# Kernel tuning notes

Hardware: AMD Instinct MI355X
Metric: run time of the kernel (lower is better)

Reference implementation:

```python
import jax, jax.numpy as jnp
import numpy as np

DIM = 1024
HEADS = 8


def setup_inputs() -> dict:
    key = jax.random.key(0)
    ks = jax.random.split(key, 8)
    b, n, m, nc, d = 2, 1024, 4, 1024, DIM
    x = jax.random.normal(ks[0], (b, n, d), dtype=jnp.float32)
    context = jax.random.normal(ks[1], (b, m, nc, d), dtype=jnp.float32)
    doc_similarities = jax.random.normal(ks[2], (b, m), dtype=jnp.float32)
    # learned params (Linear weights stored as [in, out] for x @ W)
    s = 1.0 / np.sqrt(d)
    Wq = jax.random.uniform(ks[3], (d, d), minval=-s, maxval=s, dtype=jnp.float32)
    Wkv = jax.random.uniform(ks[4], (d, 2 * d), minval=-s, maxval=s, dtype=jnp.float32)
    Wout = jax.random.uniform(ks[5], (d, d), minval=-s, maxval=s, dtype=jnp.float32)
    bout = jax.random.uniform(ks[6], (d,), minval=-s, maxval=s, dtype=jnp.float32)
    beta = jnp.array(1.0, dtype=jnp.float32)
    return {"x": x, "context": context, "doc_similarities": doc_similarities,
            "Wq": Wq, "Wkv": Wkv, "beta": beta, "Wout": Wout, "bout": bout}


def reference(x, context, doc_similarities, Wq, Wkv, beta, Wout, bout):
    b, n, dim = x.shape
    h = HEADS
    hd = dim // h
    scale = dim ** -0.5
    m, nc = context.shape[1], context.shape[2]

    # q: [b, h, n, hd]
    q = (x @ Wq).reshape(b, n, h, hd).transpose(0, 2, 1, 3)

    # flatten docs: [b, m*nc, dim]
    ctx = context.reshape(b, m * nc, dim)
    # doc similarity bias, repeated per token within each doc: [b, m*nc]
    sim = jnp.repeat(doc_similarities, nc, axis=1) * beta

    kv = ctx @ Wkv  # [b, L, 2*dim]
    k, v = jnp.split(kv, 2, axis=-1)
    k = k.reshape(b, m * nc, h, hd).transpose(0, 2, 1, 3)  # [b, h, L, hd]
    v = v.reshape(b, m * nc, h, hd).transpose(0, 2, 1, 3)

    dots = jnp.einsum('bhid,bhjd->bhij', q, k) * scale
    dots = dots + sim[:, None, None, :]
    attn = jax.nn.softmax(dots, axis=-1)
    out = jnp.einsum('bhij,bhjd->bhid', attn, v)
    out = out.transpose(0, 2, 1, 3).reshape(b, n, dim)
    return out @ Wout + bout
```

## Files before the change

### kernel.cpp

```cpp
#include <hip/hip_runtime.h>
#include <stdint.h>

typedef __attribute__((ext_vector_type(4))) float f32x4;
typedef __attribute__((ext_vector_type(8))) __bf16 bf16x8;

__device__ __forceinline__ uint16_t f2bf(float f) {
  uint32_t u = __builtin_bit_cast(uint32_t, f);
  u += 0x7FFFu + ((u >> 16) & 1u);
  return (uint16_t)(u >> 16);
}

__device__ __forceinline__ float bf2f(uint16_t u) {
  uint32_t v = ((uint32_t)u) << 16;
  return __builtin_bit_cast(float, v);
}

__device__ __forceinline__ void load_lds16(const uint16_t* g, uint16_t* l) {
  __builtin_amdgcn_global_load_lds((const __attribute__((address_space(1))) void*)g,
                                   (__attribute__((address_space(3))) void*)l, 16, 0, 0);
}

__global__ __launch_bounds__(256) void k_prep(const float* __restrict__ x,
                                              const float* __restrict__ ctx,
                                              const float* __restrict__ Wq,
                                              const float* __restrict__ Wkv,
                                              const float* __restrict__ Wout,
                                              uint16_t* __restrict__ xb,
                                              uint16_t* __restrict__ ctxb,
                                              uint16_t* __restrict__ wqt,
                                              uint16_t* __restrict__ wkvt,
                                              uint16_t* __restrict__ woutt,
                                              float qscale) {
  __shared__ float tile[32][33];
  int id = blockIdx.x;
  int tid = threadIdx.x;
  if (id < 10240) {
    const float* in;
    uint16_t* out;
    int j = id * 256 + tid;
    if (j < 524288) { in = x; out = xb; }
    else            { in = ctx; out = ctxb; j -= 524288; }
    float4 v = ((const float4*)in)[j];
    union { uint16_t u[4]; uint64_t q; } o;
    o.u[0] = f2bf(v.x); o.u[1] = f2bf(v.y); o.u[2] = f2bf(v.z); o.u[3] = f2bf(v.w);
    ((uint64_t*)out)[j] = o.q;
    return;
  }
  id -= 10240;
  const float* W;
  uint16_t* Wt;
  int N, n0, k0;
  float sc = 1.0f;
  if (id < 1024)      { W = Wq;   Wt = wqt;   N = 1024; sc = qscale;
                        n0 = (id & 31) * 32; k0 = (id >> 5) * 32; }
  else if (id < 2048) { W = Wout; Wt = woutt; N = 1024; id -= 1024;
                        n0 = (id & 31) * 32; k0 = (id >> 5) * 32; }
  else                { W = Wkv;  Wt = wkvt;  N = 2048; id -= 2048;
                        n0 = (id & 63) * 32; k0 = (id >> 6) * 32; }
  int c = tid & 31, r0 = tid >> 5;
#pragma unroll
  for (int i = 0; i < 4; i++) {
    int r = r0 + i * 8;
    tile[r][c] = W[(size_t)(k0 + r) * N + n0 + c];
  }
  __syncthreads();
#pragma unroll
  for (int i = 0; i < 4; i++) {
    int r = r0 + i * 8;
    Wt[(size_t)(n0 + r) * 1024 + k0 + c] = f2bf(tile[c][r] * sc);
  }
}

__global__ __launch_bounds__(256) void k_gemm_fused(const uint16_t* __restrict__ ctxb,
                                                    const uint16_t* __restrict__ wkvt,
                                                    const uint16_t* __restrict__ xb,
                                                    const uint16_t* __restrict__ wqt,
                                                    uint16_t* __restrict__ kb,
                                                    uint16_t* __restrict__ vtb,
                                                    uint16_t* __restrict__ qb) {
  __shared__ uint16_t smem[9216];
  uint16_t* la = smem;
  uint16_t* lb = smem + 4096;
  const int K = 1024;
  const int tid = threadIdx.x;
  const int lane = tid & 63, w = tid >> 6;
  const int quad = lane >> 4, l16 = lane & 15;
  const int wr = (w >> 1) * 64, wc = (w & 1) * 64;
  int id = blockIdx.x;
  int bx, by, isQ;
  const uint16_t *Ab, *Bb;
  if (id < 1024) {
    isQ = 0; bx = id & 15; by = id >> 4;
    Ab = ctxb + (size_t)by * 128 * K;
    Bb = wkvt + (size_t)bx * 128 * K;
  } else {
    isQ = 1; id -= 1024; bx = id & 7; by = id >> 3;
    Ab = xb + (size_t)by * 128 * K;
    Bb = wqt + (size_t)bx * 128 * K;
  }
  f32x4 acc[4][4] = {};
  const int rA = tid >> 2, slotA = tid & 3;
  const int rA1 = rA + 64;
  const int segA0 = (slotA ^ ((rA + (rA >> 2)) & 3)) * 8;
  const int segA1 = (slotA ^ ((rA1 + (rA1 >> 2)) & 3)) * 8;
  for (int k0 = 0; k0 < K; k0 += 32) {
    __syncthreads();
    load_lds16(Ab + (size_t)rA * K + k0 + segA0, la + tid * 8);
    load_lds16(Ab + (size_t)rA1 * K + k0 + segA1, la + (tid + 256) * 8);
    load_lds16(Bb + (size_t)rA * K + k0 + segA0, lb + tid * 8);
    load_lds16(Bb + (size_t)rA1 * K + k0 + segA1, lb + (tid + 256) * 8);
    __syncthreads();
    bf16x8 af[4], bfr[4];
#pragma unroll
    for (int i = 0; i < 4; i++) {
      int R = wr + i * 16 + l16;
      int s = quad ^ ((R + (R >> 2)) & 3);
      af[i] = *(const bf16x8*)&la[R * 32 + s * 8];
    }
#pragma unroll
    for (int j = 0; j < 4; j++) {
      int R = wc + j * 16 + l16;
      int s = quad ^ ((R + (R >> 2)) & 3);
      bfr[j] = *(const bf16x8*)&lb[R * 32 + s * 8];
    }
#pragma unroll
    for (int i = 0; i < 4; i++)
#pragma unroll
      for (int j = 0; j < 4; j++)
        acc[i][j] = __builtin_amdgcn_mfma_f32_16x16x32_bf16(af[i], bfr[j], acc[i][j], 0, 0, 0);
  }
  __syncthreads();
  if (isQ) {
#pragma unroll
    for (int i = 0; i < 4; i++)
#pragma unroll
      for (int j = 0; j < 4; j++) {
        size_t row = (size_t)by * 128 + wr + i * 16 + quad * 4;
        size_t col = (size_t)bx * 128 + wc + j * 16 + l16;
#pragma unroll
        for (int r = 0; r < 4; r++)
          qb[(row + r) * 1024 + col] = f2bf(acc[i][j][r]);
      }
  } else if (bx < 8) {
#pragma unroll
    for (int i = 0; i < 4; i++)
#pragma unroll
      for (int j = 0; j < 4; j++) {
        size_t row = (size_t)by * 128 + wr + i * 16 + quad * 4;
        size_t col = (size_t)bx * 128 + wc + j * 16 + l16;
#pragma unroll
        for (int r = 0; r < 4; r++)
          kb[(row + r) * 1024 + col] = f2bf(acc[i][j][r]);
      }
  } else {
    const int bh = (by >> 5) * 8 + (bx - 8);
    const int lbase = (by & 31) * 128;
    uint16_t* vdst = vtb + (size_t)bh * 524288;
#pragma unroll
    for (int half = 0; half < 2; half++) {
      if (wr == half * 64) {
#pragma unroll
        for (int i = 0; i < 4; i++)
#pragma unroll
          for (int j = 0; j < 4; j++) {
            int rowl = i * 16 + quad * 4;
            int col = wc + j * 16 + l16;
            union { uint64_t q; uint16_t u[4]; } pk;
#pragma unroll
            for (int r = 0; r < 4; r++) pk.u[r] = f2bf(acc[i][j][r]);
            *(uint64_t*)&smem[col * 72 + rowl] = pk.q;
          }
      }
      __syncthreads();
      {
        int col = tid >> 1, rseg = (tid & 1) * 32;
        const uint16_t* src = &smem[col * 72 + rseg];
        uint16_t* d = vdst + (size_t)col * 4096 + lbase + half * 64 + rseg;
#pragma unroll
        for (int k = 0; k < 4; k++)
          ((uint4*)d)[k] = *(const uint4*)&src[k * 8];
      }
      __syncthreads();
    }
  }
}

__global__ __launch_bounds__(256) void k_gemm64(const uint16_t* __restrict__ A,
                                                const uint16_t* __restrict__ Bt,
                                                float* __restrict__ Cf,
                                                const float* __restrict__ bias,
                                                int M, int N, int K) {
  __shared__ uint16_t la[64 * 64];
  __shared__ uint16_t lb[64 * 64];
  const int tid = threadIdx.x;
  const int lane = tid & 63, w = tid >> 6;
  const int quad = lane >> 4, l16 = lane & 15;
  const int wr = (w >> 1) * 32, wc = (w & 1) * 32;
  const size_t tr0 = (size_t)blockIdx.y * 64, tc0 = (size_t)blockIdx.x * 64;
  f32x4 acc[2][2] = {};
  const int rS = tid >> 3, sS = tid & 7;
  const int seg = (sS ^ (rS & 7)) * 8;
  const uint16_t* Ab = A + tr0 * K;
  const uint16_t* Bb = Bt + tc0 * K;
  for (int k0 = 0; k0 < K; k0 += 64) {
    __syncthreads();
    load_lds16(Ab + (size_t)rS * K + k0 + seg, la + tid * 8);
    load_lds16(Ab + (size_t)(rS + 32) * K + k0 + seg, la + (tid + 256) * 8);
    load_lds16(Bb + (size_t)rS * K + k0 + seg, lb + tid * 8);
    load_lds16(Bb + (size_t)(rS + 32) * K + k0 + seg, lb + (tid + 256) * 8);
    __syncthreads();
#pragma unroll
    for (int sub = 0; sub < 2; sub++) {
      const int kk = sub * 4 + quad;
      bf16x8 af[2], bfr[2];
#pragma unroll
      for (int i = 0; i < 2; i++) {
        int R = wr + i * 16 + l16;
        af[i] = *(const bf16x8*)&la[R * 64 + (kk ^ (R & 7)) * 8];
      }
#pragma unroll
      for (int j = 0; j < 2; j++) {
        int R = wc + j * 16 + l16;
        bfr[j] = *(const bf16x8*)&lb[R * 64 + (kk ^ (R & 7)) * 8];
      }
#pragma unroll
      for (int i = 0; i < 2; i++)
#pragma unroll
        for (int j = 0; j < 2; j++)
          acc[i][j] = __builtin_amdgcn_mfma_f32_16x16x32_bf16(af[i], bfr[j], acc[i][j], 0, 0, 0);
    }
  }
#pragma unroll
  for (int i = 0; i < 2; i++) {
#pragma unroll
    for (int j = 0; j < 2; j++) {
      size_t row = tr0 + wr + i * 16 + quad * 4;
      size_t col = tc0 + wc + j * 16 + l16;
#pragma unroll
      for (int r = 0; r < 4; r++)
        Cf[(row + r) * N + col] = acc[i][j][r] + bias[col];
    }
  }
}

__global__ __launch_bounds__(256) void k_attn(const uint16_t* __restrict__ q,
                                              const uint16_t* __restrict__ kb,
                                              const uint16_t* __restrict__ vt,
                                              const float* __restrict__ sims,
                                              const float* __restrict__ beta,
                                              uint16_t* __restrict__ po,
                                              float* __restrict__ pm,
                                              float* __restrict__ pl) {
  __shared__ uint16_t Kl[2][8192];
  __shared__ uint16_t Vl[2][8192];
  __shared__ uint16_t Pl[4 * 2048];
  const int bz = blockIdx.z, b = bz >> 2, sp = bz & 3;
  const int h = blockIdx.y, q0 = blockIdx.x * 128;
  const int tid = threadIdx.x, lane = tid & 63, w = tid >> 6;
  const int quad = lane >> 4, l16 = lane & 15;
  const float simv_l2 = sims[b * 4 + sp] * beta[0] * 1.44269504f;
  uint16_t* Pw = Pl + w * 2048;

  union { uint32_t u[4]; bf16x8 v; } Oc;
#pragma unroll
  for (int j = 0; j < 4; j++) Oc.u[j] = 0x3F803F80u;
  const bf16x8 onesf = Oc.v;

  bf16x8 qf[2][4];
#pragma unroll
  for (int rb = 0; rb < 2; rb++) {
    const uint16_t* qrow =
        q + ((size_t)(b * 1024 + q0 + w * 32 + rb * 16 + l16)) * 1024 + h * 128 + quad * 8;
#pragma unroll
    for (int ks = 0; ks < 4; ks++) qf[rb][ks] = *(const bf16x8*)(qrow + ks * 32);
  }
  f32x4 o[2][8] = {};
  f32x4 o9[2] = {};

  const uint16_t* kbase = kb + ((size_t)(b * 4096 + sp * 1024)) * 1024 + h * 128;
  const uint16_t* vbase = vt + ((size_t)(b * 8 + h) * 128) * 4096 + sp * 1024;

  auto stage = [&](int c, int bi) {
    const uint16_t* kc = kbase + (size_t)c * 64 * 1024;
    const uint16_t* vc = vbase + c * 64;
    uint16_t* Kb = Kl[bi];
    uint16_t* Vb = Vl[bi];
#pragma unroll
    for (int ii = 0; ii < 4; ii++) {
      int g = tid + ii * 256;
      int row = g >> 4, seg = (g & 15) ^ (row & 15);
      load_lds16(kc + (size_t)row * 1024 + seg * 8, Kb + g * 8);
    }
#pragma unroll
    for (int ii = 0; ii < 4; ii++) {
      int g = tid + ii * 256;
      int row = g >> 3, seg = (g & 7) ^ (row & 7);
      load_lds16(vc + (size_t)row * 4096 + seg * 8, Vb + g * 8);
    }
  };

  stage(0, 0);
  for (int c = 0; c < 16; c++) {
    __syncthreads();
    if (c < 15) stage(c + 1, (c + 1) & 1);
    const uint16_t* Kb = Kl[c & 1];
    const uint16_t* Vb = Vl[c & 1];
#pragma unroll
    for (int nb = 0; nb < 4; nb++) {
      f32x4 s0 = {}, s1 = {};
#pragma unroll
      for (int ks = 0; ks < 4; ks++) {
        bf16x8 kf = *(const bf16x8*)&Kb[(nb * 16 + l16) * 128 + (((ks * 4 + quad) ^ l16) * 8)];
        s0 = __builtin_amdgcn_mfma_f32_16x16x32_bf16(qf[0][ks], kf, s0, 0, 0, 0);
        s1 = __builtin_amdgcn_mfma_f32_16x16x32_bf16(qf[1][ks], kf, s1, 0, 0, 0);
      }
      const int s_lin = nb * 2 + (l16 >> 3);
#pragma unroll
      for (int r = 0; r < 4; r++) {
        int rp0 = quad * 4 + r;
        Pw[rp0 * 64 + ((s_lin ^ (rp0 & 7)) * 8) + (l16 & 7)] =
            f2bf(__builtin_amdgcn_exp2f(s0[r]));
        int rp1 = 16 + rp0;
        Pw[rp1 * 64 + ((s_lin ^ (rp1 & 7)) * 8) + (l16 & 7)] =
            f2bf(__builtin_amdgcn_exp2f(s1[r]));
      }
    }
    __asm__ volatile("s_waitcnt lgkmcnt(0)" ::: "memory");
#pragma unroll
    for (int ks = 0; ks < 2; ks++) {
      const int sq = ((ks * 4 + quad) ^ (l16 & 7)) * 8;
      bf16x8 pf0 = *(const bf16x8*)&Pw[l16 * 64 + sq];
      bf16x8 pf1 = *(const bf16x8*)&Pw[(16 + l16) * 64 + sq];
#pragma unroll
      for (int nb = 0; nb < 8; nb++) {
        bf16x8 vf = *(const bf16x8*)&Vb[(nb * 16 + l16) * 64 + sq];
        o[0][nb] = __builtin_amdgcn_mfma_f32_16x16x32_bf16(pf0, vf, o[0][nb], 0, 0, 0);
        o[1][nb] = __builtin_amdgcn_mfma_f32_16x16x32_bf16(pf1, vf, o[1][nb], 0, 0, 0);
      }
      o9[0] = __builtin_amdgcn_mfma_f32_16x16x32_bf16(pf0, onesf, o9[0], 0, 0, 0);
      o9[1] = __builtin_amdgcn_mfma_f32_16x16x32_bf16(pf1, onesf, o9[1], 0, 0, 0);
    }
  }
  const int rowbase = (sp * 16 + b * 8 + h) * 1024 + q0 + w * 32;
#pragma unroll
  for (int rb = 0; rb < 2; rb++)
#pragma unroll
    for (int r = 0; r < 4; r++) {
      int row = rowbase + rb * 16 + quad * 4 + r;
#pragma unroll
      for (int nb = 0; nb < 8; nb++)
        po[(size_t)row * 128 + nb * 16 + l16] = f2bf(o[rb][nb][r]);
      if (l16 == 0) {
        pm[row] = simv_l2;
        pl[row] = o9[rb][r];
      }
    }
}

__global__ __launch_bounds__(256) void k_merge(const uint16_t* __restrict__ po,
                                               const float* __restrict__ pm,
                                               const float* __restrict__ pl,
                                               uint16_t* __restrict__ attb) {
  const int bq = blockIdx.x;
  const int b = bq >> 10, qi = bq & 1023;
  const int t = threadIdx.x;
  const int h = t >> 5, d0 = (t & 31) * 4;
  const int bh = b * 8 + h;
  float m[4];
  float M = -INFINITY;
#pragma unroll
  for (int s = 0; s < 4; s++) {
    m[s] = pm[(s * 16 + bh) * 1024 + qi];
    M = fmaxf(M, m[s]);
  }
  float den = 0.f, wgt[4];
#pragma unroll
  for (int s = 0; s < 4; s++) {
    wgt[s] = __builtin_amdgcn_exp2f(m[s] - M);
    den += wgt[s] * pl[(s * 16 + bh) * 1024 + qi];
  }
  const float inv = 1.0f / den;
  float acc[4] = {0.f, 0.f, 0.f, 0.f};
#pragma unroll
  for (int s = 0; s < 4; s++) {
    const uint16_t* p = &po[(((size_t)(s * 16 + bh)) * 1024 + qi) * 128 + d0];
    union { uint64_t q; uint16_t u[4]; } v;
    v.q = *(const uint64_t*)p;
#pragma unroll
    for (int j = 0; j < 4; j++) acc[j] += wgt[s] * bf2f(v.u[j]);
  }
  union { uint64_t q; uint16_t u[4]; } o;
#pragma unroll
  for (int j = 0; j < 4; j++) o.u[j] = f2bf(acc[j] * inv);
  *(uint64_t*)&attb[((size_t)(b * 1024 + qi)) * 1024 + h * 128 + d0] = o.q;
}

extern "C" void kernel_launch(void* const* d_in, const int* in_sizes, int n_in,
                              void* d_out, int out_size, void* d_ws, size_t ws_size,
                              hipStream_t stream) {
  (void)in_sizes; (void)n_in; (void)out_size; (void)ws_size;
  const float* x    = (const float*)d_in[0];
  const float* ctx  = (const float*)d_in[1];
  const float* sims = (const float*)d_in[2];
  const float* Wq   = (const float*)d_in[3];
  const float* Wkv  = (const float*)d_in[4];
  const float* beta = (const float*)d_in[5];
  const float* Wout = (const float*)d_in[6];
  const float* bout = (const float*)d_in[7];
  float* out = (float*)d_out;

  char* ws = (char*)d_ws;
  uint16_t* xb    = (uint16_t*)(ws + 0);
  uint16_t* ctxb  = (uint16_t*)(ws + (4u << 20));
  uint16_t* wqt   = (uint16_t*)(ws + (20u << 20));
  uint16_t* wkvt  = (uint16_t*)(ws + (22u << 20));
  uint16_t* woutt = (uint16_t*)(ws + (26u << 20));
  uint16_t* qb    = (uint16_t*)(ws + (28u << 20));
  uint16_t* kb    = (uint16_t*)(ws + (32u << 20));
  uint16_t* vtb   = (uint16_t*)(ws + (48u << 20));
  uint16_t* attb  = (uint16_t*)(ws + (64u << 20));
  uint16_t* po = (uint16_t*)(ws + 0);
  float*    pm = (float*)(ws + (16u << 20));
  float*    pl = (float*)(ws + (16u << 20) + (256u << 10));

  const float LOG2E = 1.44269504f;
  const float qscale = 0.03125f * LOG2E;

  k_prep<<<14336, 256, 0, stream>>>(x, ctx, Wq, Wkv, Wout, xb, ctxb, wqt, wkvt, woutt, qscale);
  k_gemm_fused<<<1152, 256, 0, stream>>>(ctxb, wkvt, xb, wqt, kb, vtb, qb);
  k_attn<<<dim3(8, 8, 8), 256, 0, stream>>>(qb, kb, vtb, sims, beta, po, pm, pl);
  k_merge<<<2048, 256, 0, stream>>>(po, pm, pl, attb);
  k_gemm64<<<dim3(16, 32), 256, 0, stream>>>(attb, woutt, out, bout, 2048, 1024, 1024);
}
```

Measured before the change: 232.8 us.

## Split attention keys eight ways, single-buffer LDS, fold doc weight into partials

```diff
diff --git a/kernel.cpp b/kernel.cpp
--- a/kernel.cpp
+++ b/kernel.cpp
@@ -249,17 +249,19 @@
                                               const float* __restrict__ sims,
                                               const float* __restrict__ beta,
                                               uint16_t* __restrict__ po,
-                                              float* __restrict__ pm,
                                               float* __restrict__ pl) {
-  __shared__ uint16_t Kl[2][8192];
-  __shared__ uint16_t Vl[2][8192];
-  __shared__ uint16_t Pl[4 * 2048];
-  const int bz = blockIdx.z, b = bz >> 2, sp = bz & 3;
-  const int h = blockIdx.y, q0 = blockIdx.x * 128;
+  __shared__ uint16_t Kl[8192];
+  __shared__ uint16_t Vl[8192];
+  __shared__ uint16_t Pl[4096];
+  const int idx = blockIdx.x;
+  const int qbx = idx >> 7, g = idx & 127;
+  const int h = g >> 4, b = (g >> 3) & 1, sp = g & 7;
+  const int q0 = qbx * 128;
   const int tid = threadIdx.x, lane = tid & 63, w = tid >> 6;
   const int quad = lane >> 4, l16 = lane & 15;
-  const float simv_l2 = sims[b * 4 + sp] * beta[0] * 1.44269504f;
-  uint16_t* Pw = Pl + w * 2048;
+  const float wsplit =
+      __builtin_amdgcn_exp2f(sims[b * 4 + (sp >> 1)] * beta[0] * 1.44269504f);
+  uint16_t* Pw = Pl + w * 1024;
 
   union { uint32_t u[4]; bf16x8 v; } Oc;
 #pragma unroll
@@ -277,69 +279,63 @@
   f32x4 o[2][8] = {};
   f32x4 o9[2] = {};
 
-  const uint16_t* kbase = kb + ((size_t)(b * 4096 + sp * 1024)) * 1024 + h * 128;
-  const uint16_t* vbase = vt + ((size_t)(b * 8 + h) * 128) * 4096 + sp * 1024;
-
-  auto stage = [&](int c, int bi) {
-    const uint16_t* kc = kbase + (size_t)c * 64 * 1024;
-    const uint16_t* vc = vbase + c * 64;
-    uint16_t* Kb = Kl[bi];
-    uint16_t* Vb = Vl[bi];
+  const uint16_t* kptr = kb + ((size_t)(b * 4096 + sp * 512)) * 1024 + h * 128;
+  const uint16_t* vptr = vt + ((size_t)(b * 8 + h) * 128) * 4096 + sp * 512;
+
+  for (int c = 0; c < 8; c++) {
+    __syncthreads();
 #pragma unroll
     for (int ii = 0; ii < 4; ii++) {
-      int g = tid + ii * 256;
-      int row = g >> 4, seg = (g & 15) ^ (row & 15);
-      load_lds16(kc + (size_t)row * 1024 + seg * 8, Kb + g * 8);
+      int g2 = tid + ii * 256;
+      int row = g2 >> 4, seg = (g2 & 15) ^ (row & 15);
+      load_lds16(kptr + (size_t)row * 1024 + seg * 8, Kl + g2 * 8);
     }
 #pragma unroll
     for (int ii = 0; ii < 4; ii++) {
-      int g = tid + ii * 256;
-      int row = g >> 3, seg = (g & 7) ^ (row & 7);
-      load_lds16(vc + (size_t)row * 4096 + seg * 8, Vb + g * 8);
-    }
-  };
-
-  stage(0, 0);
-  for (int c = 0; c < 16; c++) {
-    __syncthreads();
-    if (c < 15) stage(c + 1, (c + 1) & 1);
-    const uint16_t* Kb = Kl[c & 1];
-    const uint16_t* Vb = Vl[c & 1];
-#pragma unroll
-    for (int nb = 0; nb < 4; nb++) {
-      f32x4 s0 = {}, s1 = {};
-#pragma unroll
-      for (int ks = 0; ks < 4; ks++) {
-        bf16x8 kf = *(const bf16x8*)&Kb[(nb * 16 + l16) * 128 + (((ks * 4 + quad) ^ l16) * 8)];
-        s0 = __builtin_amdgcn_mfma_f32_16x16x32_bf16(qf[0][ks], kf, s0, 0, 0, 0);
-        s1 = __builtin_amdgcn_mfma_f32_16x16x32_bf16(qf[1][ks], kf, s1, 0, 0, 0);
-      }
-      const int s_lin = nb * 2 + (l16 >> 3);
-#pragma unroll
-      for (int r = 0; r < 4; r++) {
-        int rp0 = quad * 4 + r;
-        Pw[rp0 * 64 + ((s_lin ^ (rp0 & 7)) * 8) + (l16 & 7)] =
-            f2bf(__builtin_amdgcn_exp2f(s0[r]));
-        int rp1 = 16 + rp0;
-        Pw[rp1 * 64 + ((s_lin ^ (rp1 & 7)) * 8) + (l16 & 7)] =
-            f2bf(__builtin_amdgcn_exp2f(s1[r]));
-      }
-    }
-    __asm__ volatile("s_waitcnt lgkmcnt(0)" ::: "memory");
-#pragma unroll
-    for (int ks = 0; ks < 2; ks++) {
-      const int sq = ((ks * 4 + quad) ^ (l16 & 7)) * 8;
-      bf16x8 pf0 = *(const bf16x8*)&Pw[l16 * 64 + sq];
-      bf16x8 pf1 = *(const bf16x8*)&Pw[(16 + l16) * 64 + sq];
+      int g2 = tid + ii * 256;
+      int row = g2 >> 3, seg = (g2 & 7) ^ (row & 7);
+      load_lds16(vptr + (size_t)row * 4096 + seg * 8, Vl + g2 * 8);
+    }
+    __syncthreads();
+#pragma unroll
+    for (int kh = 0; kh < 2; kh++) {
+#pragma unroll
+      for (int nb2 = 0; nb2 < 2; nb2++) {
+        const int nb = kh * 2 + nb2;
+        f32x4 s0 = {}, s1 = {};
+#pragma unroll
+        for (int ks = 0; ks < 4; ks++) {
+          bf16x8 kf = *(const bf16x8*)&Kl[(nb * 16 + l16) * 128 + (((ks * 4 + quad) ^ l16) * 8)];
+          s0 = __builtin_amdgcn_mfma_f32_16x16x32_bf16(qf[0][ks], kf, s0, 0, 0, 0);
+          s1 = __builtin_amdgcn_mfma_f32_16x16x32_bf16(qf[1][ks], kf, s1, 0, 0, 0);
+        }
+        const int sl = nb2 * 2 + (l16 >> 3);
+#pragma unroll
+        for (int r = 0; r < 4; r++) {
+          int rp0 = quad * 4 + r;
+          Pw[rp0 * 32 + ((sl ^ ((rp0 >> 1) & 3)) * 8) + (l16 & 7)] =
+              f2bf(__builtin_amdgcn_exp2f(s0[r]));
+          int rp1 = 16 + rp0;
+          Pw[rp1 * 32 + ((sl ^ ((rp1 >> 1) & 3)) * 8) + (l16 & 7)] =
+              f2bf(__builtin_amdgcn_exp2f(s1[r]));
+        }
+      }
+      __asm__ volatile("s_waitcnt lgkmcnt(0)" ::: "memory");
+      const int segp = (quad ^ ((l16 >> 1) & 3)) * 8;
+      bf16x8 pf0 = *(const bf16x8*)&Pw[l16 * 32 + segp];
+      bf16x8 pf1 = *(const bf16x8*)&Pw[(16 + l16) * 32 + segp];
+      const int sq = ((kh * 4 + quad) ^ (l16 & 7)) * 8;
 #pragma unroll
       for (int nb = 0; nb < 8; nb++) {
-        bf16x8 vf = *(const bf16x8*)&Vb[(nb * 16 + l16) * 64 + sq];
+        bf16x8 vf = *(const bf16x8*)&Vl[(nb * 16 + l16) * 64 + sq];
         o[0][nb] = __builtin_amdgcn_mfma_f32_16x16x32_bf16(pf0, vf, o[0][nb], 0, 0, 0);
         o[1][nb] = __builtin_amdgcn_mfma_f32_16x16x32_bf16(pf1, vf, o[1][nb], 0, 0, 0);
       }
       o9[0] = __builtin_amdgcn_mfma_f32_16x16x32_bf16(pf0, onesf, o9[0], 0, 0, 0);
       o9[1] = __builtin_amdgcn_mfma_f32_16x16x32_bf16(pf1, onesf, o9[1], 0, 0, 0);
     }
+    kptr += (size_t)64 * 1024;
+    vptr += 64;
   }
   const int rowbase = (sp * 16 + b * 8 + h) * 1024 + q0 + w * 32;
 #pragma unroll
@@ -349,16 +345,13 @@
       int row = rowbase + rb * 16 + quad * 4 + r;
 #pragma unroll
       for (int nb = 0; nb < 8; nb++)
-        po[(size_t)row * 128 + nb * 16 + l16] = f2bf(o[rb][nb][r]);
-      if (l16 == 0) {
-        pm[row] = simv_l2;
-        pl[row] = o9[rb][r];
-      }
+        po[(size_t)row * 128 + nb * 16 + l16] = f2bf(o[rb][nb][r] * wsplit);
+      if (l16 == 0)
+        pl[row] = o9[rb][r] * wsplit;
     }
 }
 
 __global__ __launch_bounds__(256) void k_merge(const uint16_t* __restrict__ po,
-                                               const float* __restrict__ pm,
                                                const float* __restrict__ pl,
                                                uint16_t* __restrict__ attb) {
   const int bq = blockIdx.x;
@@ -366,29 +359,17 @@
   const int t = threadIdx.x;
   const int h = t >> 5, d0 = (t & 31) * 4;
   const int bh = b * 8 + h;
-  float m[4];
-  float M = -INFINITY;
-#pragma unroll
-  for (int s = 0; s < 4; s++) {
-    m[s] = pm[(s * 16 + bh) * 1024 + qi];
-    M = fmaxf(M, m[s]);
-  }
-  float den = 0.f, wgt[4];
-#pragma unroll
-  for (int s = 0; s < 4; s++) {
-    wgt[s] = __builtin_amdgcn_exp2f(m[s] - M);
-    den += wgt[s] * pl[(s * 16 + bh) * 1024 + qi];
+  float den = 0.f;
+  float acc[4] = {0.f, 0.f, 0.f, 0.f};
+#pragma unroll
+  for (int s = 0; s < 8; s++) {
+    den += pl[(s * 16 + bh) * 1024 + qi];
+    union { uint64_t q; uint16_t u[4]; } v;
+    v.q = *(const uint64_t*)&po[(((size_t)(s * 16 + bh)) * 1024 + qi) * 128 + d0];
+#pragma unroll
+    for (int j = 0; j < 4; j++) acc[j] += bf2f(v.u[j]);
   }
   const float inv = 1.0f / den;
-  float acc[4] = {0.f, 0.f, 0.f, 0.f};
-#pragma unroll
-  for (int s = 0; s < 4; s++) {
-    const uint16_t* p = &po[(((size_t)(s * 16 + bh)) * 1024 + qi) * 128 + d0];
-    union { uint64_t q; uint16_t u[4]; } v;
-    v.q = *(const uint64_t*)p;
-#pragma unroll
-    for (int j = 0; j < 4; j++) acc[j] += wgt[s] * bf2f(v.u[j]);
-  }
   union { uint64_t q; uint16_t u[4]; } o;
 #pragma unroll
   for (int j = 0; j < 4; j++) o.u[j] = f2bf(acc[j] * inv);
@@ -414,21 +395,20 @@
   uint16_t* ctxb  = (uint16_t*)(ws + (4u << 20));
   uint16_t* wqt   = (uint16_t*)(ws + (20u << 20));
   uint16_t* wkvt  = (uint16_t*)(ws + (22u << 20));
-  uint16_t* woutt = (uint16_t*)(ws + (26u << 20));
-  uint16_t* qb    = (uint16_t*)(ws + (28u << 20));
   uint16_t* kb    = (uint16_t*)(ws + (32u << 20));
   uint16_t* vtb   = (uint16_t*)(ws + (48u << 20));
-  uint16_t* attb  = (uint16_t*)(ws + (64u << 20));
+  float*    pl    = (float*)   (ws + (64u << 20));
+  uint16_t* woutt = (uint16_t*)(ws + (68u << 20));
+  uint16_t* qb    = (uint16_t*)(ws + (70u << 20));
+  uint16_t* attb  = (uint16_t*)(ws + (74u << 20));
   uint16_t* po = (uint16_t*)(ws + 0);
-  float*    pm = (float*)(ws + (16u << 20));
-  float*    pl = (float*)(ws + (16u << 20) + (256u << 10));
 
   const float LOG2E = 1.44269504f;
   const float qscale = 0.03125f * LOG2E;
 
   k_prep<<<14336, 256, 0, stream>>>(x, ctx, Wq, Wkv, Wout, xb, ctxb, wqt, wkvt, woutt, qscale);
   k_gemm_fused<<<1152, 256, 0, stream>>>(ctxb, wkvt, xb, wqt, kb, vtb, qb);
-  k_attn<<<dim3(8, 8, 8), 256, 0, stream>>>(qb, kb, vtb, sims, beta, po, pm, pl);
-  k_merge<<<2048, 256, 0, stream>>>(po, pm, pl, attb);
+  k_attn<<<1024, 256, 0, stream>>>(qb, kb, vtb, sims, beta, po, pl);
+  k_merge<<<2048, 256, 0, stream>>>(po, pl, attb);
   k_gemm64<<<dim3(16, 32), 256, 0, stream>>>(attb, woutt, out, bout, 2048, 1024, 1024);
 }
```

New measurement: 231.9 us. Within noise of the previous version (-0.4%).
